# Optimization experiments

Measured on AMD Instinct MI355X. Metric: run time of the kernel, lower is better.

The kernel has to match this reference:

```python
import jax, jax.numpy as jnp
import numpy as np

N = 100000      # nodes
E = 3200000     # edges (avg degree 32)
D_IN = 128      # input feature dim
H = 16          # hidden_size = GCN in/out channels
M = 16          # memory_size
SLOPE = 0.01    # F.leaky_relu default negative slope


def setup_inputs() -> dict:
    key = jax.random.key(0)
    ks = jax.random.split(key, 24)
    def p(i, shape):
        return jax.random.normal(ks[i], shape, dtype=jnp.float32) * 0.05
    return {
        "x": jax.random.normal(ks[0], (N, D_IN), dtype=jnp.float32),
        "edge_index": jax.random.randint(ks[1], (2, E), 0, N),
        # preprocess Linears (torch Linear: y = x @ W.T + b)
        "W1": p(2, (256, D_IN)), "b1": p(3, (256,)),
        "W2": p(4, (H, 256)),    "b2": p(5, (H,)),
        # EvolveGNN_O layer 1: memory buffer (zeros), GRU, weight_transform, GCN bias
        "mem1": jnp.zeros((M,), jnp.float32),
        "g1_Wih": p(6, (3 * M, M)), "g1_Whh": p(7, (3 * M, M)),
        "g1_bih": p(8, (3 * M,)),   "g1_bhh": p(9, (3 * M,)),
        "wt1_W": p(10, (H * H, M)), "wt1_b": p(11, (H * H,)),
        "gcn1_b": p(12, (H,)),
        # EvolveGNN_O layer 2
        "mem2": jnp.zeros((M,), jnp.float32),
        "g2_Wih": p(13, (3 * M, M)), "g2_Whh": p(14, (3 * M, M)),
        "g2_bih": p(15, (3 * M,)),   "g2_bhh": p(16, (3 * M,)),
        "wt2_W": p(17, (H * H, M)), "wt2_b": p(18, (H * H,)),
        "gcn2_b": p(19, (H,)),
        # postprocessing Linear(hidden, 2)
        "Wout": p(20, (2, H)), "bout": p(21, (2,)),
    }


def _leaky(x):
    return jnp.where(x >= 0, x, SLOPE * x)


def _gru_step(x, Wih, Whh, bih, bhh):
    # PyTorch nn.GRU single step, h0 = 0 (default when h not provided)
    h = jnp.zeros_like(x)
    gi = Wih @ x + bih
    gh = Whh @ h + bhh
    ir, iz, inn = jnp.split(gi, 3)
    hr, hz, hn = jnp.split(gh, 3)
    r = jax.nn.sigmoid(ir + hr)
    z = jax.nn.sigmoid(iz + hz)
    n = jnp.tanh(inn + r * hn)
    return (1.0 - z) * n + z * h


def _gcn(h, row, col, W, bias):
    # PyG GCNConv: linear transform, symmetric gcn_norm (self-loops already
    # appended to row/col), gather from row, scatter-add to col, add bias.
    n = h.shape[0]
    xl = h @ W.T                                          # [N, H]
    ones = jnp.ones(row.shape[0], h.dtype)
    deg = jax.ops.segment_sum(ones, col, num_segments=n)  # in-degree incl. self-loop
    dis = jnp.where(deg > 0, jax.lax.rsqrt(deg), 0.0)
    norm = dis[row] * dis[col]                            # [E + N]
    out = jax.ops.segment_sum(xl[row] * norm[:, None], col, num_segments=n)
    return out + bias


def _evolve_gcn(h, row, col, mem, Wih, Whh, bih, bhh, wtW, wtb, gcn_b):
    new_mem = _gru_step(mem, Wih, Whh, bih, bhh)          # GRU-updated memory
    Wnew = (wtW @ new_mem + wtb).reshape(H, H)            # regenerated lin.weight [out, in]
    return _gcn(h, row, col, Wnew, gcn_b)


def reference(x, edge_index, W1, b1, W2, b2,
              mem1, g1_Wih, g1_Whh, g1_bih, g1_bhh, wt1_W, wt1_b, gcn1_b,
              mem2, g2_Wih, g2_Whh, g2_bih, g2_bhh, wt2_W, wt2_b, gcn2_b,
              Wout, bout):
    n = x.shape[0]
    loops = jnp.arange(n, dtype=edge_index.dtype)
    row = jnp.concatenate([edge_index[0], loops])         # sources (+ self-loops)
    col = jnp.concatenate([edge_index[1], loops])         # targets (+ self-loops)

    h = _leaky(x @ W1.T + b1)                             # [N, 256]
    h = _leaky(h @ W2.T + b2)                             # [N, 16]
    h = _leaky(_evolve_gcn(h, row, col, mem1, g1_Wih, g1_Whh, g1_bih, g1_bhh, wt1_W, wt1_b, gcn1_b))
    h = _leaky(_evolve_gcn(h, row, col, mem2, g2_Wih, g2_Whh, g2_bih, g2_bhh, wt2_W, wt2_b, gcn2_b))
    h = h @ Wout.T + bout                                 # [N, 2]
    return jnp.sum(h, axis=-1)                            # [N]
```

## Files before the change

### kernel.cpp

```cpp
#include <hip/hip_runtime.h>
#include <math.h>

#define SLOPE 0.01f
#define BKS   256
#define BSH2  8
#define NBKMAX 512
#define BCAP  10240

typedef short  bf16x8 __attribute__((ext_vector_type(8)));
typedef float  f32x4  __attribute__((ext_vector_type(4)));

__device__ __forceinline__ float lrelu(float v) { return v >= 0.f ? v : SLOPE * v; }

__device__ __forceinline__ unsigned short f2bf(float v) {
    unsigned u = __float_as_uint(v);
    return (unsigned short)((u + 0x7FFFu + ((u >> 16) & 1u)) >> 16);
}
__device__ __forceinline__ float bf2f(unsigned short b) {
    return __uint_as_float(((unsigned)b) << 16);
}

__global__ void prep_k(const float* __restrict__ m1, const float* __restrict__ Wih1,
                       const float* __restrict__ bih1, const float* __restrict__ bhh1,
                       const float* __restrict__ m2, const float* __restrict__ Wih2,
                       const float* __restrict__ bih2, const float* __restrict__ bhh2,
                       const float* __restrict__ wtW1, const float* __restrict__ wtb1,
                       const float* __restrict__ wtW2, const float* __restrict__ wtb2,
                       const float* __restrict__ Wout, const float* __restrict__ bout,
                       const float* __restrict__ W2, const float* __restrict__ W1,
                       float* __restrict__ Wn1, float* __restrict__ Wn2,
                       float* __restrict__ wsum, float* __restrict__ bsum,
                       unsigned short* __restrict__ W2bh, unsigned short* __restrict__ W2bl,
                       unsigned short* __restrict__ W1h, unsigned short* __restrict__ W1l,
                       int* __restrict__ bfill, int NBK) {
    if (blockIdx.x != 0) {
        int i = (blockIdx.x - 1) * 256 + threadIdx.x;
        float v = W1[i];
        unsigned short h = f2bf(v);
        W1h[i] = h;
        W1l[i] = f2bf(v - bf2f(h));
        return;
    }
    __shared__ float nm[32];
    int t = threadIdx.x;
    if (t < 32) {
        int L = t >> 4, j = t & 15;
        const float* m   = L ? m2   : m1;
        const float* Wih = L ? Wih2 : Wih1;
        const float* bih = L ? bih2 : bih1;
        const float* bhh = L ? bhh2 : bhh1;
        float gr = bih[j], gz = bih[16 + j], gn = bih[32 + j];
        for (int k = 0; k < 16; ++k) {
            float mk = m[k];
            gr += Wih[j * 16 + k] * mk;
            gz += Wih[(16 + j) * 16 + k] * mk;
            gn += Wih[(32 + j) * 16 + k] * mk;
        }
        float r = 1.f / (1.f + expf(-(gr + bhh[j])));
        float z = 1.f / (1.f + expf(-(gz + bhh[16 + j])));
        float n = tanhf(gn + r * bhh[32 + j]);
        nm[t] = (1.f - z) * n;
    }
    __syncthreads();
    float s1 = wtb1[t], s2 = wtb2[t];
    for (int k = 0; k < 16; ++k) {
        s1 += wtW1[t * 16 + k] * nm[k];
        s2 += wtW2[t * 16 + k] * nm[16 + k];
    }
    Wn1[t] = s1;
    Wn2[t] = s2;
    for (int i = t; i < 4096; i += 256) {
        float v = W2[i];
        unsigned short h = f2bf(v);
        W2bh[i] = h;
        W2bl[i] = f2bf(v - bf2f(h));
    }
    if (t < 16) wsum[t] = Wout[t] + Wout[16 + t];
    if (t == 0) bsum[0] = bout[0] + bout[1];
    for (int i = t; i < NBK; i += 256) bfill[i] = i * BCAP;
}

__global__ __launch_bounds__(256) void bscat_k(
        const int* __restrict__ row, const int* __restrict__ col,
        int* __restrict__ bfill, unsigned* __restrict__ stage,
        int E, int NBK) {
    __shared__ int lcnt[NBKMAX];
    __shared__ int s[NBKMAX];
    __shared__ int lbase[NBKMAX];
    __shared__ unsigned ledge[4096];
    __shared__ unsigned short lbkt[4096];
    int t = threadIdx.x;
    for (int i = t; i < NBK; i += 256) lcnt[i] = 0;
    for (int j = t; j < 4096; j += 256) lbkt[j] = 0xFFFFu;
    __syncthreads();
    int base = blockIdx.x * 4096;
    int r[16], d[16], sl[16];
#pragma unroll
    for (int i = 0; i < 16; ++i) {
        int e = base + i * 256 + t;
        if (e < E) {
            r[i]  = row[e];
            d[i]  = col[e];
            sl[i] = atomicAdd(&lcnt[d[i] >> BSH2], 1);
        } else d[i] = -1;
    }
    __syncthreads();
    s[t]       = (t < NBK)       ? lcnt[t]       : 0;
    s[t + 256] = (t + 256 < NBK) ? lcnt[t + 256] : 0;
    __syncthreads();
    for (int dd = 1; dd < NBKMAX; dd <<= 1) {
        int u0 = (t >= dd)       ? s[t - dd]       : 0;
        int u1 = (t + 256 >= dd) ? s[t + 256 - dd] : 0;
        __syncthreads();
        s[t]       += u0;
        s[t + 256] += u1;
        __syncthreads();
    }
    for (int i = t; i < NBK; i += 256)
        lbase[i] = lcnt[i] ? atomicAdd(bfill + i, lcnt[i]) : 0;
    __syncthreads();
#pragma unroll
    for (int i = 0; i < 16; ++i) {
        if (d[i] >= 0) {
            int bkt = d[i] >> BSH2;
            int idx = (s[bkt] - lcnt[bkt]) + sl[i];
            ledge[idx] = ((unsigned)r[i] << 8) | (unsigned)(d[i] & (BKS - 1));
            lbkt[idx]  = (unsigned short)bkt;
        }
    }
    __syncthreads();
    for (int j = t; j < 4096; j += 256) {
        int bkt = lbkt[j];
        if (bkt != 0xFFFF)
            stage[lbase[bkt] + (j - (s[bkt] - lcnt[bkt]))] = ledge[j];
    }
}

__global__ __launch_bounds__(512) void bproc_k(
        const unsigned* __restrict__ stage, const int* __restrict__ bfill,
        int* __restrict__ off, float* __restrict__ dis,
        int* __restrict__ srcs, int N, int E, int NBK) {
    __shared__ int lh[BKS];
    __shared__ int ssc[BKS];
    __shared__ int bs[NBKMAX];
    const int b  = blockIdx.x;
    const int t  = threadIdx.x;
    bs[t] = (t < NBK) ? (bfill[t] - t * BCAP) : 0;
    __syncthreads();
    for (int d = 1; d < NBKMAX; d <<= 1) {
        int u = (t >= d) ? bs[t - d] : 0;
        __syncthreads();
        bs[t] += u;
        __syncthreads();
    }
    const int myc = bfill[b] - b * BCAP;
    const int e0  = bs[b] - myc;
    const int cnt = myc;
    const int sb  = b * BCAP;
    if (b == 0 && t == 0) off[N] = E;
    if (t < BKS) lh[t] = 0;
    __syncthreads();
    {
        int i = t;
        for (; i + 1536 < cnt; i += 2048) {
            unsigned v0 = stage[sb + i];
            unsigned v1 = stage[sb + i + 512];
            unsigned v2 = stage[sb + i + 1024];
            unsigned v3 = stage[sb + i + 1536];
            atomicAdd(&lh[v0 & (BKS - 1)], 1);
            atomicAdd(&lh[v1 & (BKS - 1)], 1);
            atomicAdd(&lh[v2 & (BKS - 1)], 1);
            atomicAdd(&lh[v3 & (BKS - 1)], 1);
        }
        for (; i < cnt; i += 512)
            atomicAdd(&lh[stage[sb + i] & (BKS - 1)], 1);
    }
    __syncthreads();
    int c = (t < BKS) ? lh[t] : 0;
    if (t < BKS) ssc[t] = c;
    __syncthreads();
    for (int d = 1; d < BKS; d <<= 1) {
        int u = (t >= d && t < BKS) ? ssc[t - d] : 0;
        __syncthreads();
        if (t < BKS) ssc[t] += u;
        __syncthreads();
    }
    if (t < BKS) {
        int ex = ssc[t] - c;
        int node = b * BKS + t;
        if (node < N) {
            off[node] = e0 + ex;
            dis[node] = rsqrtf((float)(c + 1));
        }
        lh[t] = ex;
    }
    __syncthreads();
    {
        int i = t;
        for (; i + 1536 < cnt; i += 2048) {
            unsigned v0 = stage[sb + i];
            unsigned v1 = stage[sb + i + 512];
            unsigned v2 = stage[sb + i + 1024];
            unsigned v3 = stage[sb + i + 1536];
            int p0 = e0 + atomicAdd(&lh[v0 & (BKS - 1)], 1);
            int p1 = e0 + atomicAdd(&lh[v1 & (BKS - 1)], 1);
            int p2 = e0 + atomicAdd(&lh[v2 & (BKS - 1)], 1);
            int p3 = e0 + atomicAdd(&lh[v3 & (BKS - 1)], 1);
            srcs[p0] = (int)(v0 >> 8);
            srcs[p1] = (int)(v1 >> 8);
            srcs[p2] = (int)(v2 >> 8);
            srcs[p3] = (int)(v3 >> 8);
        }
        for (; i < cnt; i += 512) {
            unsigned v = stage[sb + i];
            int pos = e0 + atomicAdd(&lh[v & (BKS - 1)], 1);
            srcs[pos] = (int)(v >> 8);
        }
    }
}

__global__ __launch_bounds__(512, 4) void mlp_k(
        const float* __restrict__ x,
        const unsigned short* __restrict__ W1h,
        const unsigned short* __restrict__ W1l,
        const float* __restrict__ b1,
        const unsigned short* __restrict__ W2bh,
        const unsigned short* __restrict__ W2bl,
        const float* __restrict__ b2,
        const float* __restrict__ Wn1,
        const float* __restrict__ dis,
        unsigned short* __restrict__ xl, int N) {
    __shared__ float sbuf[11008];
    unsigned short* xh  = (unsigned short*)sbuf;
    unsigned short* xlo = xh + 8704;
    unsigned short* h1h = (unsigned short*)sbuf;
    float*          h2p = sbuf + 8448;

    const int t      = threadIdx.x;
    const int nl     = t & 63;
    const int q      = __builtin_amdgcn_readfirstlane(t >> 6);
    const int lane15 = t & 15;
    const int quad   = (t & 63) >> 4;
    const int node   = blockIdx.x * 64 + nl;
    const bool valid = node < N;

    {
        const float4* x4 = (const float4*)x;
        const size_t tb = (size_t)blockIdx.x * 2048;
        unsigned* xh32 = (unsigned*)xh;
        unsigned* xl32 = (unsigned*)xlo;
#pragma unroll
        for (int kk = 0; kk < 4; ++kk) {
            int idx  = kk * 512 + t;
            int row  = idx >> 5;
            int col4 = idx & 31;
            float4 v = make_float4(0.f, 0.f, 0.f, 0.f);
            if (blockIdx.x * 64 + row < N) v = x4[tb + idx];
            unsigned short hx = f2bf(v.x), hy = f2bf(v.y);
            unsigned short hz = f2bf(v.z), hw = f2bf(v.w);
            unsigned short lx = f2bf(v.x - bf2f(hx)), ly = f2bf(v.y - bf2f(hy));
            unsigned short lz = f2bf(v.z - bf2f(hz)), lw = f2bf(v.w - bf2f(hw));
            int base = row * 68 + col4 * 2;
            *(uint2*)(xh32 + base) =
                make_uint2((unsigned)hx | ((unsigned)hy << 16),
                           (unsigned)hz | ((unsigned)hw << 16));
            *(uint2*)(xl32 + base) =
                make_uint2((unsigned)lx | ((unsigned)ly << 16),
                           (unsigned)lz | ((unsigned)lw << 16));
        }
    }
    __syncthreads();

    f32x4 acc[4][2];
#pragma unroll
    for (int mt = 0; mt < 4; ++mt)
#pragma unroll
        for (int nt = 0; nt < 2; ++nt)
            acc[mt][nt] = (f32x4){0.f, 0.f, 0.f, 0.f};

#pragma unroll
    for (int nt = 0; nt < 2; ++nt) {
        bf16x8 bh[4], bl[4];
#pragma unroll
        for (int ks = 0; ks < 4; ++ks) {
            size_t wo = (size_t)(q * 32 + nt * 16 + lane15) * 128 + ks * 32 + quad * 8;
            bh[ks] = *(const bf16x8*)(W1h + wo);
            bl[ks] = *(const bf16x8*)(W1l + wo);
        }
#pragma unroll
        for (int ks = 0; ks < 4; ++ks) {
            const int koff = ks * 32 + quad * 8;
#pragma unroll
            for (int mt = 0; mt < 4; ++mt) {
                bf16x8 ah = *(const bf16x8*)(xh  + (16 * mt + lane15) * 136 + koff);
                bf16x8 al = *(const bf16x8*)(xlo + (16 * mt + lane15) * 136 + koff);
                acc[mt][nt] = __builtin_amdgcn_mfma_f32_16x16x32_bf16(ah, bh[ks], acc[mt][nt], 0, 0, 0);
                acc[mt][nt] = __builtin_amdgcn_mfma_f32_16x16x32_bf16(ah, bl[ks], acc[mt][nt], 0, 0, 0);
                acc[mt][nt] = __builtin_amdgcn_mfma_f32_16x16x32_bf16(al, bh[ks], acc[mt][nt], 0, 0, 0);
            }
        }
    }
    __syncthreads();

    const int kh  = q >> 2;
    const int mt2 = q & 3;
    bf16x8 w2hf[4], w2lf[4];
#pragma unroll
    for (int ks2 = 0; ks2 < 4; ++ks2) {
        int wo = lane15 * 256 + (kh * 4 + ks2) * 32 + quad * 8;
        w2hf[ks2] = *(const bf16x8*)(W2bh + wo);
        w2lf[ks2] = *(const bf16x8*)(W2bl + wo);
    }

#pragma unroll
    for (int nt = 0; nt < 2; ++nt) {
        int hu = q * 32 + nt * 16 + lane15;
        float bb = b1[hu];
#pragma unroll
        for (int mt = 0; mt < 4; ++mt) {
            int row0 = 16 * mt + quad * 4;
#pragma unroll
            for (int r = 0; r < 4; ++r) {
                float v = lrelu(acc[mt][nt][r] + bb);
                h1h[(row0 + r) * 264 + hu] = f2bf(v);
            }
        }
    }
    __syncthreads();

    f32x4 a2 = (f32x4){0.f, 0.f, 0.f, 0.f};
#pragma unroll
    for (int ks2 = 0; ks2 < 4; ++ks2) {
        const int koff = (kh * 4 + ks2) * 32 + quad * 8;
        bf16x8 ah = *(const bf16x8*)(h1h + (16 * mt2 + lane15) * 264 + koff);
        a2 = __builtin_amdgcn_mfma_f32_16x16x32_bf16(ah, w2hf[ks2], a2, 0, 0, 0);
        a2 = __builtin_amdgcn_mfma_f32_16x16x32_bf16(ah, w2lf[ks2], a2, 0, 0, 0);
    }
    {
        float* dst = h2p + kh * 1280 + (16 * mt2 + quad * 4) * 20 + lane15;
        dst[0] = a2[0]; dst[20] = a2[1]; dst[40] = a2[2]; dst[60] = a2[3];
    }
    __syncthreads();

    {
        const f32x4* pa = (const f32x4*)(h2p + nl * 20);
        const f32x4* pb = (const f32x4*)(h2p + 1280 + nl * 20);
        f32x4 s[4];
#pragma unroll
        for (int i = 0; i < 4; ++i) s[i] = pa[i] + pb[i];
        float o0 = 0.f, o1 = 0.f;
        const float* wr0 = Wn1 + (2 * q) * 16;
        const float* wr1 = Wn1 + (2 * q + 1) * 16;
#pragma unroll
        for (int j = 0; j < 16; ++j) {
            float h = lrelu(s[j >> 2][j & 3] + b2[j]);
            o0 = fmaf(wr0[j], h, o0);
            o1 = fmaf(wr1[j], h, o1);
        }
        if (valid) {
            float d = dis[node];
            unsigned pk = (unsigned)f2bf(d * o0) | ((unsigned)f2bf(d * o1) << 16);
            *(unsigned*)(xl + (size_t)node * 16 + 2 * q) = pk;
        }
    }
}

__global__ void gather1_k(const int* __restrict__ off, const int* __restrict__ srcs,
                          const float* __restrict__ dis,
                          const unsigned short* __restrict__ xin,
                          const float* __restrict__ bias, const float* __restrict__ Wn2,
                          unsigned short* __restrict__ xout, int N) {
    __shared__ float w[256];
    {
        int j = threadIdx.x >> 4, c = threadIdx.x & 15;
        w[threadIdx.x] = Wn2[c * 16 + j];
    }
    __syncthreads();
    int g = blockIdx.x * 16 + (threadIdx.x >> 4);
    int c = threadIdx.x & 15;
    if (g >= N) return;
    float acc = bf2f(xin[(size_t)g * 16 + c]);
    int e  = off[g];
    int e1 = off[g + 1];
    for (; e + 15 < e1; e += 16) {
        int ss[16];
#pragma unroll
        for (int i = 0; i < 16; ++i) ss[i] = srcs[e + i];
        float vv[16];
#pragma unroll
        for (int i = 0; i < 16; ++i) vv[i] = bf2f(xin[(size_t)ss[i] * 16 + c]);
        float p0 = (vv[0] + vv[1]) + (vv[2] + vv[3]);
        float p1 = (vv[4] + vv[5]) + (vv[6] + vv[7]);
        float p2 = (vv[8] + vv[9]) + (vv[10] + vv[11]);
        float p3 = (vv[12] + vv[13]) + (vv[14] + vv[15]);
        acc += (p0 + p1) + (p2 + p3);
    }
    for (; e + 7 < e1; e += 8) {
        int s0 = srcs[e],     s1 = srcs[e + 1], s2 = srcs[e + 2], s3 = srcs[e + 3];
        int s4 = srcs[e + 4], s5 = srcs[e + 5], s6 = srcs[e + 6], s7 = srcs[e + 7];
        float v0 = bf2f(xin[(size_t)s0 * 16 + c]);
        float v1 = bf2f(xin[(size_t)s1 * 16 + c]);
        float v2 = bf2f(xin[(size_t)s2 * 16 + c]);
        float v3 = bf2f(xin[(size_t)s3 * 16 + c]);
        float v4 = bf2f(xin[(size_t)s4 * 16 + c]);
        float v5 = bf2f(xin[(size_t)s5 * 16 + c]);
        float v6 = bf2f(xin[(size_t)s6 * 16 + c]);
        float v7 = bf2f(xin[(size_t)s7 * 16 + c]);
        acc += ((v0 + v1) + (v2 + v3)) + ((v4 + v5) + (v6 + v7));
    }
    for (; e < e1; ++e)
        acc += bf2f(xin[(size_t)srcs[e] * 16 + c]);
    float d = dis[g];
    float h = lrelu(fmaf(d, acc, bias[c]));
    float o = 0.f;
#pragma unroll
    for (int j = 0; j < 16; ++j) o = fmaf(w[j * 16 + c], __shfl(h, j, 16), o);
    xout[(size_t)g * 16 + c] = f2bf(d * o);
}

__global__ void gather2_k(const int* __restrict__ off, const int* __restrict__ srcs,
                          const float* __restrict__ dis,
                          const unsigned short* __restrict__ xin,
                          const float* __restrict__ bias, const float* __restrict__ wsum,
                          const float* __restrict__ bsum, float* __restrict__ out, int N) {
    int g = blockIdx.x * 16 + (threadIdx.x >> 4);
    int c = threadIdx.x & 15;
    if (g >= N) return;
    float acc = bf2f(xin[(size_t)g * 16 + c]);
    int e  = off[g];
    int e1 = off[g + 1];
    for (; e + 15 < e1; e += 16) {
        int ss[16];
#pragma unroll
        for (int i = 0; i < 16; ++i) ss[i] = srcs[e + i];
        float vv[16];
#pragma unroll
        for (int i = 0; i < 16; ++i) vv[i] = bf2f(xin[(size_t)ss[i] * 16 + c]);
        float p0 = (vv[0] + vv[1]) + (vv[2] + vv[3]);
        float p1 = (vv[4] + vv[5]) + (vv[6] + vv[7]);
        float p2 = (vv[8] + vv[9]) + (vv[10] + vv[11]);
        float p3 = (vv[12] + vv[13]) + (vv[14] + vv[15]);
        acc += (p0 + p1) + (p2 + p3);
    }
    for (; e + 7 < e1; e += 8) {
        int s0 = srcs[e],     s1 = srcs[e + 1], s2 = srcs[e + 2], s3 = srcs[e + 3];
        int s4 = srcs[e + 4], s5 = srcs[e + 5], s6 = srcs[e + 6], s7 = srcs[e + 7];
        float v0 = bf2f(xin[(size_t)s0 * 16 + c]);
        float v1 = bf2f(xin[(size_t)s1 * 16 + c]);
        float v2 = bf2f(xin[(size_t)s2 * 16 + c]);
        float v3 = bf2f(xin[(size_t)s3 * 16 + c]);
        float v4 = bf2f(xin[(size_t)s4 * 16 + c]);
        float v5 = bf2f(xin[(size_t)s5 * 16 + c]);
        float v6 = bf2f(xin[(size_t)s6 * 16 + c]);
        float v7 = bf2f(xin[(size_t)s7 * 16 + c]);
        acc += ((v0 + v1) + (v2 + v3)) + ((v4 + v5) + (v6 + v7));
    }
    for (; e < e1; ++e)
        acc += bf2f(xin[(size_t)srcs[e] * 16 + c]);
    float v = wsum[c] * lrelu(fmaf(dis[g], acc, bias[c]));
#pragma unroll
    for (int m = 1; m < 16; m <<= 1) v += __shfl_xor(v, m);
    if (c == 0) out[g] = v + bsum[0];
}

extern "C" void kernel_launch(void* const* d_in, const int* in_sizes, int n_in,
                              void* d_out, int out_size, void* d_ws, size_t ws_size,
                              hipStream_t stream) {
    const float* x      = (const float*)d_in[0];
    const int*   edge   = (const int*)d_in[1];
    const float* W1     = (const float*)d_in[2];
    const float* b1     = (const float*)d_in[3];
    const float* W2     = (const float*)d_in[4];
    const float* b2     = (const float*)d_in[5];
    const float* mem1   = (const float*)d_in[6];
    const float* g1_Wih = (const float*)d_in[7];
    const float* g1_bih = (const float*)d_in[9];
    const float* g1_bhh = (const float*)d_in[10];
    const float* wt1_W  = (const float*)d_in[11];
    const float* wt1_b  = (const float*)d_in[12];
    const float* gcn1_b = (const float*)d_in[13];
    const float* mem2   = (const float*)d_in[14];
    const float* g2_Wih = (const float*)d_in[15];
    const float* g2_bih = (const float*)d_in[17];
    const float* g2_bhh = (const float*)d_in[18];
    const float* wt2_W  = (const float*)d_in[19];
    const float* wt2_b  = (const float*)d_in[20];
    const float* gcn2_b = (const float*)d_in[21];
    const float* Wout   = (const float*)d_in[22];
    const float* bout   = (const float*)d_in[23];
    float* out = (float*)d_out;

    const int N = in_sizes[0] / 128;
    const int E = in_sizes[1] / 2;
    const int* row = edge;
    const int* col = edge + E;

    const int NBK = (N + BKS - 1) >> BSH2;
    const int gM  = (N + 63) / 64;
    const int gG  = (N + 15) / 16;
    const int gB  = (E + 4095) / 4096;

    float* ws    = (float*)d_ws;
    float* bufA  = ws;
    float* bufB  = bufA + (size_t)N * 16;
    float* dis   = bufB + (size_t)N * 16;
    float* sm    = dis + N;
    float* Wn1   = sm;
    float* Wn2   = sm + 256;
    float* wsum  = sm + 512;
    float* bsum  = sm + 528;
    unsigned short* W2bh = (unsigned short*)(sm + 544);
    unsigned short* W2bl = (unsigned short*)(sm + 2592);
    unsigned short* W1h = (unsigned short*)(sm + 4640);
    unsigned short* W1l = (unsigned short*)(sm + 21024);
    int*   bfill = (int*)(sm + 37408);
    int*   bbase2= bfill + NBKMAX;
    int*   off   = bbase2 + NBKMAX + 1;
    int*   srcs  = off + N + 1;
    size_t stoff = (size_t)(srcs + E - (int*)d_ws);
    stoff = (stoff + 3) & ~(size_t)3;
    unsigned* stage = (unsigned*)((int*)d_ws + stoff);

    prep_k<<<129, 256, 0, stream>>>(mem1, g1_Wih, g1_bih, g1_bhh,
                                    mem2, g2_Wih, g2_bih, g2_bhh,
                                    wt1_W, wt1_b, wt2_W, wt2_b,
                                    Wout, bout, W2, W1, Wn1, Wn2, wsum, bsum,
                                    W2bh, W2bl, W1h, W1l, bfill, NBK);
    bscat_k<<<gB, 256, 0, stream>>>(row, col, bfill, stage, E, NBK);
    bproc_k<<<NBK, 512, 0, stream>>>(stage, bfill, off, dis, srcs, N, E, NBK);
    mlp_k<<<gM, 512, 0, stream>>>(x, W1h, W1l, b1, W2bh, W2bl, b2, Wn1, dis,
                                  (unsigned short*)bufA, N);
    gather1_k<<<gG, 256, 0, stream>>>(off, srcs, dis, (unsigned short*)bufA,
                                      gcn1_b, Wn2, (unsigned short*)bufB, N);
    gather2_k<<<gG, 256, 0, stream>>>(off, srcs, dis, (unsigned short*)bufB,
                                      gcn2_b, wsum, bsum, out, N);
}
```

Baseline: 301.8 us.

## Count in-degree with global atomics and prefetch next x tile in MLP

```diff
diff --git a/kernel.cpp b/kernel.cpp
--- a/kernel.cpp
+++ b/kernel.cpp
@@ -32,7 +32,10 @@
                        float* __restrict__ wsum, float* __restrict__ bsum,
                        unsigned short* __restrict__ W2bh, unsigned short* __restrict__ W2bl,
                        unsigned short* __restrict__ W1h, unsigned short* __restrict__ W1l,
-                       int* __restrict__ bfill, int NBK) {
+                       int* __restrict__ bfill, int* __restrict__ ncnt,
+                       int NBK, int N) {
+    for (int i = blockIdx.x * 256 + threadIdx.x; i < N; i += gridDim.x * 256)
+        ncnt[i] = 0;
     if (blockIdx.x != 0) {
         int i = (blockIdx.x - 1) * 256 + threadIdx.x;
         float v = W1[i];
@@ -83,7 +86,7 @@
 __global__ __launch_bounds__(256) void bscat_k(
         const int* __restrict__ row, const int* __restrict__ col,
         int* __restrict__ bfill, unsigned* __restrict__ stage,
-        int E, int NBK) {
+        int* __restrict__ ncnt, int E, int NBK) {
     __shared__ int lcnt[NBKMAX];
     __shared__ int s[NBKMAX];
     __shared__ int lbase[NBKMAX];
@@ -102,6 +105,7 @@
             r[i]  = row[e];
             d[i]  = col[e];
             sl[i] = atomicAdd(&lcnt[d[i] >> BSH2], 1);
+            atomicAdd(&ncnt[d[i]], 1);
         } else d[i] = -1;
     }
     __syncthreads();
@@ -138,6 +142,7 @@
 
 __global__ __launch_bounds__(512) void bproc_k(
         const unsigned* __restrict__ stage, const int* __restrict__ bfill,
+        const int* __restrict__ ncnt,
         int* __restrict__ off, float* __restrict__ dis,
         int* __restrict__ srcs, int N, int E, int NBK) {
     __shared__ int lh[BKS];
@@ -158,26 +163,12 @@
     const int cnt = myc;
     const int sb  = b * BCAP;
     if (b == 0 && t == 0) off[N] = E;
-    if (t < BKS) lh[t] = 0;
-    __syncthreads();
-    {
-        int i = t;
-        for (; i + 1536 < cnt; i += 2048) {
-            unsigned v0 = stage[sb + i];
-            unsigned v1 = stage[sb + i + 512];
-            unsigned v2 = stage[sb + i + 1024];
-            unsigned v3 = stage[sb + i + 1536];
-            atomicAdd(&lh[v0 & (BKS - 1)], 1);
-            atomicAdd(&lh[v1 & (BKS - 1)], 1);
-            atomicAdd(&lh[v2 & (BKS - 1)], 1);
-            atomicAdd(&lh[v3 & (BKS - 1)], 1);
-        }
-        for (; i < cnt; i += 512)
-            atomicAdd(&lh[stage[sb + i] & (BKS - 1)], 1);
-    }
-    __syncthreads();
-    int c = (t < BKS) ? lh[t] : 0;
-    if (t < BKS) ssc[t] = c;
+    const int node = b * BKS + t;
+    int c = 0;
+    if (t < BKS) {
+        c = (node < N) ? ncnt[node] : 0;
+        ssc[t] = c;
+    }
     __syncthreads();
     for (int d = 1; d < BKS; d <<= 1) {
         int u = (t >= d && t < BKS) ? ssc[t - d] : 0;
@@ -187,7 +178,6 @@
     }
     if (t < BKS) {
         int ex = ssc[t] - c;
-        int node = b * BKS + t;
         if (node < N) {
             off[node] = e0 + ex;
             dis[node] = rsqrtf((float)(c + 1));
@@ -241,66 +231,6 @@
     const int q      = __builtin_amdgcn_readfirstlane(t >> 6);
     const int lane15 = t & 15;
     const int quad   = (t & 63) >> 4;
-    const int node   = blockIdx.x * 64 + nl;
-    const bool valid = node < N;
-
-    {
-        const float4* x4 = (const float4*)x;
-        const size_t tb = (size_t)blockIdx.x * 2048;
-        unsigned* xh32 = (unsigned*)xh;
-        unsigned* xl32 = (unsigned*)xlo;
-#pragma unroll
-        for (int kk = 0; kk < 4; ++kk) {
-            int idx  = kk * 512 + t;
-            int row  = idx >> 5;
-            int col4 = idx & 31;
-            float4 v = make_float4(0.f, 0.f, 0.f, 0.f);
-            if (blockIdx.x * 64 + row < N) v = x4[tb + idx];
-            unsigned short hx = f2bf(v.x), hy = f2bf(v.y);
-            unsigned short hz = f2bf(v.z), hw = f2bf(v.w);
-            unsigned short lx = f2bf(v.x - bf2f(hx)), ly = f2bf(v.y - bf2f(hy));
-            unsigned short lz = f2bf(v.z - bf2f(hz)), lw = f2bf(v.w - bf2f(hw));
-            int base = row * 68 + col4 * 2;
-            *(uint2*)(xh32 + base) =
-                make_uint2((unsigned)hx | ((unsigned)hy << 16),
-                           (unsigned)hz | ((unsigned)hw << 16));
-            *(uint2*)(xl32 + base) =
-                make_uint2((unsigned)lx | ((unsigned)ly << 16),
-                           (unsigned)lz | ((unsigned)lw << 16));
-        }
-    }
-    __syncthreads();
-
-    f32x4 acc[4][2];
-#pragma unroll
-    for (int mt = 0; mt < 4; ++mt)
-#pragma unroll
-        for (int nt = 0; nt < 2; ++nt)
-            acc[mt][nt] = (f32x4){0.f, 0.f, 0.f, 0.f};
-
-#pragma unroll
-    for (int nt = 0; nt < 2; ++nt) {
-        bf16x8 bh[4], bl[4];
-#pragma unroll
-        for (int ks = 0; ks < 4; ++ks) {
-            size_t wo = (size_t)(q * 32 + nt * 16 + lane15) * 128 + ks * 32 + quad * 8;
-            bh[ks] = *(const bf16x8*)(W1h + wo);
-            bl[ks] = *(const bf16x8*)(W1l + wo);
-        }
-#pragma unroll
-        for (int ks = 0; ks < 4; ++ks) {
-            const int koff = ks * 32 + quad * 8;
-#pragma unroll
-            for (int mt = 0; mt < 4; ++mt) {
-                bf16x8 ah = *(const bf16x8*)(xh  + (16 * mt + lane15) * 136 + koff);
-                bf16x8 al = *(const bf16x8*)(xlo + (16 * mt + lane15) * 136 + koff);
-                acc[mt][nt] = __builtin_amdgcn_mfma_f32_16x16x32_bf16(ah, bh[ks], acc[mt][nt], 0, 0, 0);
-                acc[mt][nt] = __builtin_amdgcn_mfma_f32_16x16x32_bf16(ah, bl[ks], acc[mt][nt], 0, 0, 0);
-                acc[mt][nt] = __builtin_amdgcn_mfma_f32_16x16x32_bf16(al, bh[ks], acc[mt][nt], 0, 0, 0);
-            }
-        }
-    }
-    __syncthreads();
 
     const int kh  = q >> 2;
     const int mt2 = q & 3;
@@ -312,56 +242,145 @@
         w2lf[ks2] = *(const bf16x8*)(W2bl + wo);
     }
 
-#pragma unroll
-    for (int nt = 0; nt < 2; ++nt) {
-        int hu = q * 32 + nt * 16 + lane15;
-        float bb = b1[hu];
-#pragma unroll
-        for (int mt = 0; mt < 4; ++mt) {
-            int row0 = 16 * mt + quad * 4;
-#pragma unroll
-            for (int r = 0; r < 4; ++r) {
-                float v = lrelu(acc[mt][nt][r] + bb);
-                h1h[(row0 + r) * 264 + hu] = f2bf(v);
-            }
-        }
-    }
-    __syncthreads();
-
-    f32x4 a2 = (f32x4){0.f, 0.f, 0.f, 0.f};
-#pragma unroll
-    for (int ks2 = 0; ks2 < 4; ++ks2) {
-        const int koff = (kh * 4 + ks2) * 32 + quad * 8;
-        bf16x8 ah = *(const bf16x8*)(h1h + (16 * mt2 + lane15) * 264 + koff);
-        a2 = __builtin_amdgcn_mfma_f32_16x16x32_bf16(ah, w2hf[ks2], a2, 0, 0, 0);
-        a2 = __builtin_amdgcn_mfma_f32_16x16x32_bf16(ah, w2lf[ks2], a2, 0, 0, 0);
-    }
+    float4 xv[4];
     {
-        float* dst = h2p + kh * 1280 + (16 * mt2 + quad * 4) * 20 + lane15;
-        dst[0] = a2[0]; dst[20] = a2[1]; dst[40] = a2[2]; dst[60] = a2[3];
-    }
-    __syncthreads();
-
-    {
-        const f32x4* pa = (const f32x4*)(h2p + nl * 20);
-        const f32x4* pb = (const f32x4*)(h2p + 1280 + nl * 20);
-        f32x4 s[4];
-#pragma unroll
-        for (int i = 0; i < 4; ++i) s[i] = pa[i] + pb[i];
-        float o0 = 0.f, o1 = 0.f;
-        const float* wr0 = Wn1 + (2 * q) * 16;
-        const float* wr1 = Wn1 + (2 * q + 1) * 16;
-#pragma unroll
-        for (int j = 0; j < 16; ++j) {
-            float h = lrelu(s[j >> 2][j & 3] + b2[j]);
-            o0 = fmaf(wr0[j], h, o0);
-            o1 = fmaf(wr1[j], h, o1);
-        }
-        if (valid) {
-            float d = dis[node];
-            unsigned pk = (unsigned)f2bf(d * o0) | ((unsigned)f2bf(d * o1) << 16);
-            *(unsigned*)(xl + (size_t)node * 16 + 2 * q) = pk;
-        }
+        const int tile = blockIdx.x * 2;
+        const float4* x4 = (const float4*)x;
+        const size_t tb = (size_t)tile * 2048;
+#pragma unroll
+        for (int kk = 0; kk < 4; ++kk) {
+            int idx = kk * 512 + t;
+            int row = idx >> 5;
+            xv[kk] = make_float4(0.f, 0.f, 0.f, 0.f);
+            if (tile * 64 + row < N) xv[kk] = x4[tb + idx];
+        }
+    }
+
+#pragma unroll
+    for (int ti = 0; ti < 2; ++ti) {
+        const int tile = blockIdx.x * 2 + ti;
+
+        {
+            unsigned* xh32 = (unsigned*)xh;
+            unsigned* xl32 = (unsigned*)xlo;
+#pragma unroll
+            for (int kk = 0; kk < 4; ++kk) {
+                int idx  = kk * 512 + t;
+                int row  = idx >> 5;
+                int col4 = idx & 31;
+                float4 v = xv[kk];
+                unsigned short hx = f2bf(v.x), hy = f2bf(v.y);
+                unsigned short hz = f2bf(v.z), hw = f2bf(v.w);
+                unsigned short lx = f2bf(v.x - bf2f(hx)), ly = f2bf(v.y - bf2f(hy));
+                unsigned short lz = f2bf(v.z - bf2f(hz)), lw = f2bf(v.w - bf2f(hw));
+                int base = row * 68 + col4 * 2;
+                *(uint2*)(xh32 + base) =
+                    make_uint2((unsigned)hx | ((unsigned)hy << 16),
+                               (unsigned)hz | ((unsigned)hw << 16));
+                *(uint2*)(xl32 + base) =
+                    make_uint2((unsigned)lx | ((unsigned)ly << 16),
+                               (unsigned)lz | ((unsigned)lw << 16));
+            }
+        }
+        __syncthreads();
+
+        if (ti == 0) {
+            const int tile1 = blockIdx.x * 2 + 1;
+            const float4* x4 = (const float4*)x;
+            const size_t tb = (size_t)tile1 * 2048;
+#pragma unroll
+            for (int kk = 0; kk < 4; ++kk) {
+                int idx = kk * 512 + t;
+                int row = idx >> 5;
+                xv[kk] = make_float4(0.f, 0.f, 0.f, 0.f);
+                if (tile1 * 64 + row < N) xv[kk] = x4[tb + idx];
+            }
+        }
+
+        f32x4 acc[4][2];
+#pragma unroll
+        for (int mt = 0; mt < 4; ++mt)
+#pragma unroll
+            for (int nt = 0; nt < 2; ++nt)
+                acc[mt][nt] = (f32x4){0.f, 0.f, 0.f, 0.f};
+
+#pragma unroll
+        for (int nt = 0; nt < 2; ++nt) {
+            bf16x8 bh[4], bl[4];
+#pragma unroll
+            for (int ks = 0; ks < 4; ++ks) {
+                size_t wo = (size_t)(q * 32 + nt * 16 + lane15) * 128 + ks * 32 + quad * 8;
+                bh[ks] = *(const bf16x8*)(W1h + wo);
+                bl[ks] = *(const bf16x8*)(W1l + wo);
+            }
+#pragma unroll
+            for (int ks = 0; ks < 4; ++ks) {
+                const int koff = ks * 32 + quad * 8;
+#pragma unroll
+                for (int mt = 0; mt < 4; ++mt) {
+                    bf16x8 ah = *(const bf16x8*)(xh  + (16 * mt + lane15) * 136 + koff);
+                    bf16x8 al = *(const bf16x8*)(xlo + (16 * mt + lane15) * 136 + koff);
+                    acc[mt][nt] = __builtin_amdgcn_mfma_f32_16x16x32_bf16(ah, bh[ks], acc[mt][nt], 0, 0, 0);
+                    acc[mt][nt] = __builtin_amdgcn_mfma_f32_16x16x32_bf16(ah, bl[ks], acc[mt][nt], 0, 0, 0);
+                    acc[mt][nt] = __builtin_amdgcn_mfma_f32_16x16x32_bf16(al, bh[ks], acc[mt][nt], 0, 0, 0);
+                }
+            }
+        }
+        __syncthreads();
+
+#pragma unroll
+        for (int nt = 0; nt < 2; ++nt) {
+            int hu = q * 32 + nt * 16 + lane15;
+            float bb = b1[hu];
+#pragma unroll
+            for (int mt = 0; mt < 4; ++mt) {
+                int row0 = 16 * mt + quad * 4;
+#pragma unroll
+                for (int r = 0; r < 4; ++r) {
+                    float v = lrelu(acc[mt][nt][r] + bb);
+                    h1h[(row0 + r) * 264 + hu] = f2bf(v);
+                }
+            }
+        }
+        __syncthreads();
+
+        f32x4 a2 = (f32x4){0.f, 0.f, 0.f, 0.f};
+#pragma unroll
+        for (int ks2 = 0; ks2 < 4; ++ks2) {
+            const int koff = (kh * 4 + ks2) * 32 + quad * 8;
+            bf16x8 ah = *(const bf16x8*)(h1h + (16 * mt2 + lane15) * 264 + koff);
+            a2 = __builtin_amdgcn_mfma_f32_16x16x32_bf16(ah, w2hf[ks2], a2, 0, 0, 0);
+            a2 = __builtin_amdgcn_mfma_f32_16x16x32_bf16(ah, w2lf[ks2], a2, 0, 0, 0);
+        }
+        {
+            float* dst = h2p + kh * 1280 + (16 * mt2 + quad * 4) * 20 + lane15;
+            dst[0] = a2[0]; dst[20] = a2[1]; dst[40] = a2[2]; dst[60] = a2[3];
+        }
+        __syncthreads();
+
+        {
+            const int node = tile * 64 + nl;
+            const f32x4* pa = (const f32x4*)(h2p + nl * 20);
+            const f32x4* pb = (const f32x4*)(h2p + 1280 + nl * 20);
+            f32x4 s[4];
+#pragma unroll
+            for (int i = 0; i < 4; ++i) s[i] = pa[i] + pb[i];
+            float o0 = 0.f, o1 = 0.f;
+            const float* wr0 = Wn1 + (2 * q) * 16;
+            const float* wr1 = Wn1 + (2 * q + 1) * 16;
+#pragma unroll
+            for (int j = 0; j < 16; ++j) {
+                float h = lrelu(s[j >> 2][j & 3] + b2[j]);
+                o0 = fmaf(wr0[j], h, o0);
+                o1 = fmaf(wr1[j], h, o1);
+            }
+            if (node < N) {
+                float d = dis[node];
+                unsigned pk = (unsigned)f2bf(d * o0) | ((unsigned)f2bf(d * o1) << 16);
+                *(unsigned*)(xl + (size_t)node * 16 + 2 * q) = pk;
+            }
+        }
+        __syncthreads();
     }
 }
 
@@ -495,10 +514,11 @@
     const int* row = edge;
     const int* col = edge + E;
 
-    const int NBK = (N + BKS - 1) >> BSH2;
-    const int gM  = (N + 63) / 64;
-    const int gG  = (N + 15) / 16;
-    const int gB  = (E + 4095) / 4096;
+    const int NBK    = (N + BKS - 1) >> BSH2;
+    const int ntiles = (N + 63) / 64;
+    const int gM     = (ntiles + 1) / 2;
+    const int gG     = (N + 15) / 16;
+    const int gB     = (E + 4095) / 4096;
 
     float* ws    = (float*)d_ws;
     float* bufA  = ws;
@@ -517,7 +537,8 @@
     int*   bbase2= bfill + NBKMAX;
     int*   off   = bbase2 + NBKMAX + 1;
     int*   srcs  = off + N + 1;
-    size_t stoff = (size_t)(srcs + E - (int*)d_ws);
+    int*   ncnt  = srcs + E;
+    size_t stoff = (size_t)(ncnt + N - (int*)d_ws);
     stoff = (stoff + 3) & ~(size_t)3;
     unsigned* stage = (unsigned*)((int*)d_ws + stoff);
 
@@ -525,9 +546,9 @@
                                     mem2, g2_Wih, g2_bih, g2_bhh,
                                     wt1_W, wt1_b, wt2_W, wt2_b,
                                     Wout, bout, W2, W1, Wn1, Wn2, wsum, bsum,
-                                    W2bh, W2bl, W1h, W1l, bfill, NBK);
-    bscat_k<<<gB, 256, 0, stream>>>(row, col, bfill, stage, E, NBK);
-    bproc_k<<<NBK, 512, 0, stream>>>(stage, bfill, off, dis, srcs, N, E, NBK);
+                                    W2bh, W2bl, W1h, W1l, bfill, ncnt, NBK, N);
+    bscat_k<<<gB, 256, 0, stream>>>(row, col, bfill, stage, ncnt, E, NBK);
+    bproc_k<<<NBK, 512, 0, stream>>>(stage, bfill, ncnt, off, dis, srcs, N, E, NBK);
     mlp_k<<<gM, 512, 0, stream>>>(x, W1h, W1l, b1, W2bh, W2bl, b2, Wn1, dis,
                                   (unsigned short*)bufA, N);
     gather1_k<<<gG, 256, 0, stream>>>(off, srcs, dis, (unsigned short*)bufA,
```

After: 466.5 us. 54.6% more time.
